# Kernel tuning notes

Measured on AMD Instinct MI355X. Metric: run time of the kernel, lower is better.

The kernel has to match this reference:

```python
import jax, jax.numpy as jnp
import numpy as np

N, E, IN_DIM, H, D, EDGE_DIM, T = 50000, 800000, 128, 4, 32, 32, 8
NEG_SLOPE = 0.2


def setup_inputs() -> dict:
    key = jax.random.key(0)
    ks = jax.random.split(key, 12)
    s = 0.1  # xavier-ish scale
    return {
        "h": jax.random.normal(ks[0], (N, IN_DIM), jnp.float32),
        "W": jax.random.normal(ks[1], (IN_DIM, D * H), jnp.float32) * s,
        "edge_emb": jax.random.normal(ks[2], (T, EDGE_DIM), jnp.float32) * s,
        "W_r": jax.random.normal(ks[3], (T, EDGE_DIM, EDGE_DIM * H), jnp.float32) * s,
        "a_l": jax.random.normal(ks[4], (1, H, D), jnp.float32) * s,
        "a_r": jax.random.normal(ks[5], (1, H, D), jnp.float32) * s,
        "a_e": jax.random.normal(ks[6], (1, H, EDGE_DIM), jnp.float32) * s,
        "res_w": jax.random.normal(ks[7], (IN_DIM, D * H), jnp.float32) * s,
        "res_b": jnp.zeros((D * H,), jnp.float32),
        "row": jax.random.randint(ks[8], (E,), 0, N),  # src node per edge
        "col": jax.random.randint(ks[9], (E,), 0, N),  # dst node per edge
        "etype": jax.random.randint(ks[10], (E,), 0, T),
    }


def reference(h, W, edge_emb, W_r, a_l, a_r, a_e, res_w, res_b, row, col, etype):
    # node projection: [N, H, D]
    emb = (h @ W).reshape(-1, H, D)

    # TypedLinear on edge-type embeddings. Since edge features depend only on
    # etype, compute the per-type result once, then gather per edge.
    e_t = jnp.einsum('te,tef->tf', edge_emb, W_r).reshape(T, H, EDGE_DIM)
    h_e_t = (a_e * e_t).sum(-1)            # [T, H]

    h_l = (a_l * emb).sum(-1)              # [N, H]
    h_r = (a_r * emb).sum(-1)              # [N, H]
    scores = h_l[row] + h_r[col] + h_e_t[etype]          # [E, H]
    scores = jax.nn.leaky_relu(scores, NEG_SLOPE)

    # segment softmax over edges sharing the same destination node (col)
    m = jax.ops.segment_max(scores, col, num_segments=N)  # [N, H]
    ex = jnp.exp(scores - m[col])
    denom = jax.ops.segment_sum(ex, col, num_segments=N)
    alpha = ex / denom[col]                # [E, H]

    # u_mul_e + scatter-sum to destination nodes
    msg = emb[row] * alpha[:, :, None]     # [E, H, D]
    agg = jax.ops.segment_sum(msg, col, num_segments=N)   # [N, H, D]

    # original permutes to [N, D, H] before flattening (d-major layout)
    out = jnp.transpose(agg, (0, 2, 1)).reshape(-1, D * H)
    out = out + h @ res_w + res_b          # residual
    return jax.nn.elu(out)
```

## Files before the change

kernel.cpp:

```cpp
#include <hip/hip_runtime.h>
#include <math.h>

#define NH 4
#define EDIM 32
#define NEG_SLOPE 0.2f
#define BSH 6
#define BCAP 2048

typedef __attribute__((ext_vector_type(8))) short short8;
typedef __attribute__((ext_vector_type(4))) float f32x4;
typedef __attribute__((ext_vector_type(2))) float f32x2;

__device__ __forceinline__ unsigned short f2bf(float f) {
    unsigned int x = __builtin_bit_cast(unsigned int, f);
    unsigned int r = (x + 0x7fffu + ((x >> 16) & 1u)) >> 16;
    return (unsigned short)r;
}
__device__ __forceinline__ float bf2f(unsigned short u) {
    unsigned int x = ((unsigned int)u) << 16;
    return __builtin_bit_cast(float, x);
}

__global__ __launch_bounds__(256) void k_prep(
    const float* __restrict__ W, const float* __restrict__ Rw,
    unsigned short* __restrict__ Wt, unsigned short* __restrict__ Rwt,
    int* __restrict__ bucket_cursor,
    const float* __restrict__ edge_emb, const float* __restrict__ W_r,
    const float* __restrict__ a_e, float* __restrict__ h_e_t)
{
    int tid = threadIdx.x;
    if (blockIdx.x < 64) {
        int idx = blockIdx.x * 256 + tid;
        int n = idx >> 7, k = idx & 127;
        Wt[n * 128 + k]  = f2bf(W[k * 128 + n]);
        Rwt[n * 128 + k] = f2bf(Rw[k * 128 + n]);
        if (idx < 1024) bucket_cursor[idx] = idx * BCAP;
    } else {
        int j = blockIdx.x - 64;
        int t = j >> 2;
        int ec = (j & 3) * 2 + (tid >> 7);
        int rem = tid & 127;
        float v = 0.f;
#pragma unroll
        for (int u = 0; u < 4; ++u) {
            int e = ec * 4 + u;
            v += edge_emb[t * EDIM + e] * W_r[(size_t)(t * EDIM + e) * 128 + rem];
        }
        v *= a_e[rem];
#pragma unroll
        for (int off = 16; off >= 1; off >>= 1)
            v += __shfl_xor(v, off);
        if ((rem & 31) == 0) atomicAdd(&h_e_t[t * NH + (rem >> 5)], v);
    }
}

__global__ __launch_bounds__(256) void k_gemm_fill(
    const float* __restrict__ A, const unsigned short* __restrict__ Wt,
    const unsigned short* __restrict__ Rwt, const float* __restrict__ Rb,
    const float* __restrict__ a_l, const float* __restrict__ a_r,
    unsigned short* __restrict__ EmbBf, unsigned short* __restrict__ ResBf,
    float* __restrict__ h_l, float* __restrict__ h_r, int M,
    const int* __restrict__ row, const int* __restrict__ col,
    const int* __restrict__ etype, int* __restrict__ bucket_cursor,
    unsigned* __restrict__ ebuf, int E, int NB, int nFill)
{
    __shared__ char lds[49152];
    int tid = threadIdx.x;

    if ((int)blockIdx.x < nFill) {
        int* bins = (int*)lds;
        int* base = bins + 1024;
        for (int i = tid; i < NB; i += 256) bins[i] = 0;
        __syncthreads();
        int lo = blockIdx.x * 8192;
        int ccol[32];
#pragma unroll
        for (int u = 0; u < 32; ++u) {
            int i = lo + tid + u * 256;
            int c = (i < E) ? col[i] : -1;
            ccol[u] = c;
            if (c >= 0) atomicAdd(&bins[c >> BSH], 1);
        }
        __syncthreads();
        for (int i = tid; i < NB; i += 256) {
            int c = bins[i];
            base[i] = c ? atomicAdd(&bucket_cursor[i], c) : 0;
            bins[i] = 0;
        }
        __syncthreads();
#pragma unroll
        for (int u = 0; u < 32; ++u) {
            int i = lo + tid + u * 256;
            int c = ccol[u];
            if (c >= 0) {
                int bk = c >> BSH;
                int p = base[bk] + atomicAdd(&bins[bk], 1);
                ebuf[p] = (unsigned)row[i] | ((unsigned)etype[i] << 16)
                        | ((unsigned)(c & 63) << 24);
            }
        }
        return;
    }

    int m0 = ((int)blockIdx.x - nFill) * 64;
#pragma unroll
    for (int i = 0; i < 4; ++i) {
        int c = tid + 256 * i;
        int r = c >> 4, kc = c & 15;
        int grow = m0 + r;
        float4 v0 = make_float4(0.f, 0.f, 0.f, 0.f), v1 = v0;
        if (grow < M) {
            v0 = *(const float4*)&A[(size_t)grow * 128 + kc * 8];
            v1 = *(const float4*)&A[(size_t)grow * 128 + kc * 8 + 4];
        }
        union { unsigned short u[8]; uint4 v; } p;
        p.u[0] = f2bf(v0.x); p.u[1] = f2bf(v0.y); p.u[2] = f2bf(v0.z); p.u[3] = f2bf(v0.w);
        p.u[4] = f2bf(v1.x); p.u[5] = f2bf(v1.y); p.u[6] = f2bf(v1.z); p.u[7] = f2bf(v1.w);
        int b = (r * 256 + kc * 16) ^ ((r & 7) << 4);
        *(uint4*)&lds[b] = p.v;
    }
#pragma unroll
    for (int i = 0; i < 8; ++i) {
        int c = tid + 256 * i;
        int n = c >> 4, kc = c & 15;
        uint4 v = *(const uint4*)&Wt[n * 128 + kc * 8];
        int b = 16384 + ((n * 256 + kc * 16) ^ ((n & 7) << 4));
        *(uint4*)&lds[b] = v;
    }
    __syncthreads();

    int w = tid >> 6, lane = tid & 63;
    int g = lane >> 4, l15 = lane & 15;
    int lrow = w * 16 + l15;

    short8 a[4];
#pragma unroll
    for (int s = 0; s < 4; ++s)
        a[s] = *(const short8*)&lds[(lrow * 256 + s * 64 + g * 16) ^ ((lrow & 7) << 4)];

    f32x4 acc[8];
#pragma unroll
    for (int f = 0; f < 8; ++f) acc[f] = (f32x4){0.f, 0.f, 0.f, 0.f};

#pragma unroll
    for (int f = 0; f < 8; ++f) {
        int n = f * 16 + l15;
        int nsw = (n & 7) << 4;
#pragma unroll
        for (int s = 0; s < 4; ++s) {
            short8 b = *(const short8*)&lds[16384 + ((n * 256 + s * 64 + g * 16) ^ nsw)];
            acc[f] = __builtin_amdgcn_mfma_f32_16x16x32_bf16(a[s], b, acc[f], 0, 0, 0);
        }
    }
#pragma unroll
    for (int f = 0; f < 8; ++f) {
        int col2 = f * 16 + l15;
#pragma unroll
        for (int reg = 0; reg < 4; ++reg) {
            int grow = m0 + w * 16 + g * 4 + reg;
            if (grow < M) EmbBf[(size_t)grow * 128 + col2] = f2bf(acc[f][reg]);
        }
    }
    {
        float alv[8], arv[8];
#pragma unroll
        for (int f = 0; f < 8; ++f) {
            alv[f] = a_l[f * 16 + l15];
            arv[f] = a_r[f * 16 + l15];
        }
#pragma unroll
        for (int reg = 0; reg < 4; ++reg) {
            float4 hl4, hr4;
#pragma unroll
            for (int hh = 0; hh < 4; ++hh) {
                float pl = alv[2 * hh] * acc[2 * hh][reg] + alv[2 * hh + 1] * acc[2 * hh + 1][reg];
                float pr = arv[2 * hh] * acc[2 * hh][reg] + arv[2 * hh + 1] * acc[2 * hh + 1][reg];
#pragma unroll
                for (int off = 8; off >= 1; off >>= 1) {
                    pl += __shfl_xor(pl, off);
                    pr += __shfl_xor(pr, off);
                }
                (&hl4.x)[hh] = pl;
                (&hr4.x)[hh] = pr;
            }
            int grow = m0 + w * 16 + g * 4 + reg;
            if (l15 == 0 && grow < M) {
                *(float4*)&h_l[(size_t)grow * 4] = hl4;
                *(float4*)&h_r[(size_t)grow * 4] = hr4;
            }
        }
    }

    __syncthreads();
#pragma unroll
    for (int i = 0; i < 8; ++i) {
        int c = tid + 256 * i;
        int n = c >> 4, kc = c & 15;
        uint4 v = *(const uint4*)&Rwt[n * 128 + kc * 8];
        int b = 16384 + ((n * 256 + kc * 16) ^ ((n & 7) << 4));
        *(uint4*)&lds[b] = v;
    }
    __syncthreads();

#pragma unroll
    for (int f = 0; f < 8; ++f) acc[f] = (f32x4){0.f, 0.f, 0.f, 0.f};
#pragma unroll
    for (int f = 0; f < 8; ++f) {
        int n = f * 16 + l15;
        int nsw = (n & 7) << 4;
#pragma unroll
        for (int s = 0; s < 4; ++s) {
            short8 b = *(const short8*)&lds[16384 + ((n * 256 + s * 64 + g * 16) ^ nsw)];
            acc[f] = __builtin_amdgcn_mfma_f32_16x16x32_bf16(a[s], b, acc[f], 0, 0, 0);
        }
    }
#pragma unroll
    for (int f = 0; f < 8; ++f) {
        int col2 = f * 16 + l15;
        float bias = Rb[col2];
#pragma unroll
        for (int reg = 0; reg < 4; ++reg) {
            int grow = m0 + w * 16 + g * 4 + reg;
            if (grow < M) ResBf[(size_t)grow * 128 + col2] = f2bf(acc[f][reg] + bias);
        }
    }
}

__global__ __launch_bounds__(512) void k_sort_aggregate(
    const unsigned* __restrict__ ebuf, const int* __restrict__ bucket_cursor,
    const float* __restrict__ h_l, const float* __restrict__ h_e_t,
    const float* __restrict__ h_r, const unsigned short* __restrict__ embBf,
    const unsigned short* __restrict__ resBf, float* __restrict__ out, int N)
{
    __shared__ int sedge[BCAP];
    __shared__ int cnt[64];
    __shared__ int scn[65];
    __shared__ char shalpha[8 * 1536];

    int b = blockIdx.x;
    int tid = threadIdx.x;
    int seg = b * BCAP;
    int m = bucket_cursor[b] - seg;

    if (tid < 64) cnt[tid] = 0;
    __syncthreads();
    for (int i = tid; i < m; i += 512)
        atomicAdd(&cnt[(ebuf[seg + i] >> 24) & 63], 1);
    __syncthreads();
    if (tid < 64) {
        int v = cnt[tid];
        int s = v;
#pragma unroll
        for (int off = 1; off < 64; off <<= 1) {
            int u2 = __shfl_up(s, off);
            if (tid >= off) s += u2;
        }
        scn[tid + 1] = s;
        if (tid == 0) scn[0] = 0;
        cnt[tid] = s - v;
    }
    __syncthreads();
    for (int i = tid; i < m; i += 512) {
        unsigned e = ebuf[seg + i];
        int p = atomicAdd(&cnt[(e >> 24) & 63], 1);
        sedge[p] = (int)(e & 0x00FFFFFFu);
    }
    __syncthreads();

    int w = tid >> 6, lane = tid & 63;
    int myh = lane >> 4;
    char* wb = &shalpha[w * 1536];
    const char* ab = wb + 256 + myh * 260;
    const char* embByte = (const char*)embBf;

    for (int it = 0; it < 8; ++it) {
        int nd = it * 8 + w;
        int n = b * 64 + nd;
        if (n >= N) break;
        int st0 = scn[nd];
        int deg = scn[nd + 1] - st0;
        float4 hrv = *(const float4*)&h_r[(size_t)n * 4];
        f32x2 acc2 = (f32x2){0.f, 0.f};

        if (deg <= 64) {
            bool act = lane < deg;
            float p0 = 0.f, p1 = 0.f, p2 = 0.f, p3 = 0.f;
            if (act) {
                int pk = sedge[st0 + lane];
                int r = pk & 0xffff;
                float4 hl = *(const float4*)&h_l[(size_t)r * 4];
                float4 he = *(const float4*)&h_e_t[(size_t)(pk >> 16) * 4];
                float sc0 = hl.x + he.x + hrv.x; sc0 = sc0 > 0.f ? sc0 : NEG_SLOPE * sc0;
                float sc1 = hl.y + he.y + hrv.y; sc1 = sc1 > 0.f ? sc1 : NEG_SLOPE * sc1;
                float sc2 = hl.z + he.z + hrv.z; sc2 = sc2 > 0.f ? sc2 : NEG_SLOPE * sc2;
                float sc3 = hl.w + he.w + hrv.w; sc3 = sc3 > 0.f ? sc3 : NEG_SLOPE * sc3;
                p0 = __expf(sc0); p1 = __expf(sc1);
                p2 = __expf(sc2); p3 = __expf(sc3);
                *(int*)(wb + lane * 4) = pk << 8 >> 8 << 8;
                *(int*)(wb + lane * 4) = (pk & 0xffff) << 8;
                *(float*)(wb + 256 + 0 * 260 + lane * 4) = p0;
                *(float*)(wb + 256 + 1 * 260 + lane * 4) = p1;
                *(float*)(wb + 256 + 2 * 260 + lane * 4) = p2;
                *(float*)(wb + 256 + 3 * 260 + lane * 4) = p3;
            }
            float d0 = p0, d1 = p1, d2 = p2, d3 = p3;
#pragma unroll
            for (int off = 32; off >= 1; off >>= 1) {
                d0 += __shfl_xor(d0, off); d1 += __shfl_xor(d1, off);
                d2 += __shfl_xor(d2, off); d3 += __shfl_xor(d3, off);
            }
            float den = myh == 0 ? d0 : myh == 1 ? d1 : myh == 2 ? d2 : d3;
            float inv = (deg > 0) ? __builtin_amdgcn_rcpf(den) : 0.f;

            int q = 0;
            for (; q + 8 <= deg; q += 8) {
                int ro[8]; float aq[8];
#pragma unroll
                for (int u = 0; u < 8; ++u) ro[u] = *(const int*)(wb + (q + u) * 4);
#pragma unroll
                for (int u = 0; u < 8; ++u) aq[u] = *(const float*)(ab + (q + u) * 4);
                unsigned int ev[8];
#pragma unroll
                for (int u = 0; u < 8; ++u)
                    ev[u] = *(const unsigned int*)(embByte + (size_t)(unsigned)(ro[u] + lane * 4));
#pragma unroll
                for (int u = 0; u < 8; ++u) {
                    f32x2 ef;
                    ef.x = __builtin_bit_cast(float, ev[u] << 16);
                    ef.y = __builtin_bit_cast(float, ev[u] & 0xffff0000u);
                    acc2 = __builtin_elementwise_fma(ef, (f32x2){aq[u], aq[u]}, acc2);
                }
            }
            for (; q < deg; ++q) {
                int ro = *(const int*)(wb + q * 4);
                float aq = *(const float*)(ab + q * 4);
                unsigned int ev = *(const unsigned int*)(embByte + (size_t)(unsigned)(ro + lane * 4));
                f32x2 ef;
                ef.x = __builtin_bit_cast(float, ev << 16);
                ef.y = __builtin_bit_cast(float, ev & 0xffff0000u);
                acc2 = __builtin_elementwise_fma(ef, (f32x2){aq, aq}, acc2);
            }
            acc2.x *= inv; acc2.y *= inv;
        } else {
            float d0 = 0.f, d1 = 0.f, d2 = 0.f, d3 = 0.f;
            for (int base2 = 0; base2 < deg; base2 += 64) {
                int el = base2 + lane;
                if (el < deg) {
                    int pk = sedge[st0 + el];
                    float4 hl = *(const float4*)&h_l[(size_t)(pk & 0xffff) * 4];
                    float4 he = *(const float4*)&h_e_t[(size_t)(pk >> 16) * 4];
                    float sc0 = hl.x + he.x + hrv.x; sc0 = sc0 > 0.f ? sc0 : NEG_SLOPE * sc0;
                    float sc1 = hl.y + he.y + hrv.y; sc1 = sc1 > 0.f ? sc1 : NEG_SLOPE * sc1;
                    float sc2 = hl.z + he.z + hrv.z; sc2 = sc2 > 0.f ? sc2 : NEG_SLOPE * sc2;
                    float sc3 = hl.w + he.w + hrv.w; sc3 = sc3 > 0.f ? sc3 : NEG_SLOPE * sc3;
                    d0 += __expf(sc0); d1 += __expf(sc1);
                    d2 += __expf(sc2); d3 += __expf(sc3);
                }
            }
#pragma unroll
            for (int off = 32; off >= 1; off >>= 1) {
                d0 += __shfl_xor(d0, off); d1 += __shfl_xor(d1, off);
                d2 += __shfl_xor(d2, off); d3 += __shfl_xor(d3, off);
            }
            float den = myh == 0 ? d0 : myh == 1 ? d1 : myh == 2 ? d2 : d3;
            float inv = __builtin_amdgcn_rcpf(den);
            for (int base2 = 0; base2 < deg; base2 += 64) {
                int el = base2 + lane;
                float p0 = 0.f, p1 = 0.f, p2 = 0.f, p3 = 0.f;
                int r = 0;
                if (el < deg) {
                    int pk = sedge[st0 + el];
                    r = pk & 0xffff;
                    float4 hl = *(const float4*)&h_l[(size_t)r * 4];
                    float4 he = *(const float4*)&h_e_t[(size_t)(pk >> 16) * 4];
                    float sc0 = hl.x + he.x + hrv.x; sc0 = sc0 > 0.f ? sc0 : NEG_SLOPE * sc0;
                    float sc1 = hl.y + he.y + hrv.y; sc1 = sc1 > 0.f ? sc1 : NEG_SLOPE * sc1;
                    float sc2 = hl.z + he.z + hrv.z; sc2 = sc2 > 0.f ? sc2 : NEG_SLOPE * sc2;
                    float sc3 = hl.w + he.w + hrv.w; sc3 = sc3 > 0.f ? sc3 : NEG_SLOPE * sc3;
                    p0 = __expf(sc0); p1 = __expf(sc1);
                    p2 = __expf(sc2); p3 = __expf(sc3);
                }
                int cmax = (deg - base2 < 64) ? (deg - base2) : 64;
                for (int qq = 0; qq < cmax; ++qq) {
                    int rq = __shfl(r, qq);
                    float a0 = __shfl(p0, qq), a1 = __shfl(p1, qq);
                    float a2 = __shfl(p2, qq), a3 = __shfl(p3, qq);
                    float aq = myh == 0 ? a0 : myh == 1 ? a1 : myh == 2 ? a2 : a3;
                    unsigned int ev = *(const unsigned int*)&embBf[(size_t)rq * 128 + lane * 2];
                    f32x2 ef;
                    ef.x = __builtin_bit_cast(float, ev << 16);
                    ef.y = __builtin_bit_cast(float, ev & 0xffff0000u);
                    acc2 = __builtin_elementwise_fma(ef, (f32x2){aq, aq}, acc2);
                }
            }
            acc2.x *= inv; acc2.y *= inv;
        }

        int j0 = lane * 2;
        int h0 = j0 >> 5, dd0 = j0 & 31;
        size_t ob = (size_t)n * 128;
        float o0 = acc2.x + bf2f(resBf[ob + dd0 * 4 + h0]);
        float o1 = acc2.y + bf2f(resBf[ob + (dd0 + 1) * 4 + h0]);
        out[ob + dd0 * 4 + h0] = o0 > 0.f ? o0 : expm1f(o0);
        out[ob + (dd0 + 1) * 4 + h0] = o1 > 0.f ? o1 : expm1f(o1);
    }
}

extern "C" void kernel_launch(void* const* d_in, const int* in_sizes, int n_in,
                              void* d_out, int out_size, void* d_ws, size_t ws_size,
                              hipStream_t stream)
{
    const float* h        = (const float*)d_in[0];
    const float* W        = (const float*)d_in[1];
    const float* edge_emb = (const float*)d_in[2];
    const float* W_r      = (const float*)d_in[3];
    const float* a_l      = (const float*)d_in[4];
    const float* a_r      = (const float*)d_in[5];
    const float* a_e      = (const float*)d_in[6];
    const float* res_w    = (const float*)d_in[7];
    const float* res_b    = (const float*)d_in[8];
    const int*   row      = (const int*)d_in[9];
    const int*   col      = (const int*)d_in[10];
    const int*   etype    = (const int*)d_in[11];
    float* out = (float*)d_out;

    int N = in_sizes[0] / 128;
    int E = in_sizes[9];
    int T = in_sizes[2] / EDIM;
    int NB = (N + 63) >> BSH;

    char* ws = (char*)d_ws;
    size_t off = 0;
    auto alloc = [&](size_t bytes) -> char* {
        char* p = ws + off;
        off = (off + bytes + 255) & ~(size_t)255;
        return p;
    };
    unsigned short* embBf = (unsigned short*)alloc((size_t)N * 128 * 2);
    unsigned short* resBf = (unsigned short*)alloc((size_t)N * 128 * 2);
    unsigned short* Wt    = (unsigned short*)alloc((size_t)128 * 128 * 2);
    unsigned short* Rwt   = (unsigned short*)alloc((size_t)128 * 128 * 2);
    float* h_l   = (float*)alloc((size_t)N * 4 * 4);
    float* h_r   = (float*)alloc((size_t)N * 4 * 4);
    float* h_e_t = (float*)alloc((size_t)T * 4 * 4);
    int* bucket_cursor = (int*)alloc(1024 * 4);
    unsigned* ebuf = (unsigned*)alloc((size_t)(NB + 1) * BCAP * 4);

    int nFill = (E + 8191) / 8192;
    int nGemm = (N + 63) / 64;

    hipMemsetAsync(h_e_t, 0, (size_t)T * NH * 4, stream);
    hipLaunchKernelGGL(k_prep, dim3(64 + T * 4), dim3(256), 0, stream,
                       W, res_w, Wt, Rwt, bucket_cursor,
                       edge_emb, W_r, a_e, h_e_t);
    hipLaunchKernelGGL(k_gemm_fill, dim3(nFill + nGemm), dim3(256), 0, stream,
                       h, Wt, Rwt, res_b, a_l, a_r, embBf, resBf, h_l, h_r, N,
                       row, col, etype, bucket_cursor, ebuf, E, NB, nFill);
    hipLaunchKernelGGL(k_sort_aggregate, dim3(NB), dim3(512), 0, stream,
                       ebuf, bucket_cursor, h_l, h_e_t, h_r, embBf, resBf, out, N);
}
```

Measured before the change: 91.89 us.

## Halve bucket size and split edge gather across half-waves with 8-byte loads

```diff
diff --git a/kernel.cpp b/kernel.cpp
--- a/kernel.cpp
+++ b/kernel.cpp
@@ -4,8 +4,8 @@
 #define NH 4
 #define EDIM 32
 #define NEG_SLOPE 0.2f
-#define BSH 6
-#define BCAP 2048
+#define BSH 5
+#define BCAP 1024
 
 typedef __attribute__((ext_vector_type(8))) short short8;
 typedef __attribute__((ext_vector_type(4))) float f32x4;
@@ -34,7 +34,7 @@
         int n = idx >> 7, k = idx & 127;
         Wt[n * 128 + k]  = f2bf(W[k * 128 + n]);
         Rwt[n * 128 + k] = f2bf(Rw[k * 128 + n]);
-        if (idx < 1024) bucket_cursor[idx] = idx * BCAP;
+        if (idx < 2048) bucket_cursor[idx] = idx * BCAP;
     } else {
         int j = blockIdx.x - 64;
         int t = j >> 2;
@@ -69,13 +69,13 @@
 
     if ((int)blockIdx.x < nFill) {
         int* bins = (int*)lds;
-        int* base = bins + 1024;
+        int* base = bins + 2048;
         for (int i = tid; i < NB; i += 256) bins[i] = 0;
         __syncthreads();
-        int lo = blockIdx.x * 8192;
-        int ccol[32];
-#pragma unroll
-        for (int u = 0; u < 32; ++u) {
+        int lo = blockIdx.x * 4096;
+        int ccol[16];
+#pragma unroll
+        for (int u = 0; u < 16; ++u) {
             int i = lo + tid + u * 256;
             int c = (i < E) ? col[i] : -1;
             ccol[u] = c;
@@ -89,14 +89,14 @@
         }
         __syncthreads();
 #pragma unroll
-        for (int u = 0; u < 32; ++u) {
+        for (int u = 0; u < 16; ++u) {
             int i = lo + tid + u * 256;
             int c = ccol[u];
             if (c >= 0) {
                 int bk = c >> BSH;
                 int p = base[bk] + atomicAdd(&bins[bk], 1);
                 ebuf[p] = (unsigned)row[i] | ((unsigned)etype[i] << 16)
-                        | ((unsigned)(c & 63) << 24);
+                        | ((unsigned)(c & 31) << 24);
             }
         }
         return;
@@ -226,32 +226,32 @@
     }
 }
 
-__global__ __launch_bounds__(512) void k_sort_aggregate(
+__global__ __launch_bounds__(256) void k_sort_aggregate(
     const unsigned* __restrict__ ebuf, const int* __restrict__ bucket_cursor,
     const float* __restrict__ h_l, const float* __restrict__ h_e_t,
     const float* __restrict__ h_r, const unsigned short* __restrict__ embBf,
     const unsigned short* __restrict__ resBf, float* __restrict__ out, int N)
 {
     __shared__ int sedge[BCAP];
-    __shared__ int cnt[64];
-    __shared__ int scn[65];
-    __shared__ char shalpha[8 * 1536];
+    __shared__ int cnt[32];
+    __shared__ int scn[33];
+    __shared__ char shalpha[4 * 1536];
 
     int b = blockIdx.x;
     int tid = threadIdx.x;
     int seg = b * BCAP;
     int m = bucket_cursor[b] - seg;
 
-    if (tid < 64) cnt[tid] = 0;
-    __syncthreads();
-    for (int i = tid; i < m; i += 512)
-        atomicAdd(&cnt[(ebuf[seg + i] >> 24) & 63], 1);
-    __syncthreads();
-    if (tid < 64) {
+    if (tid < 32) cnt[tid] = 0;
+    __syncthreads();
+    for (int i = tid; i < m; i += 256)
+        atomicAdd(&cnt[(ebuf[seg + i] >> 24) & 31], 1);
+    __syncthreads();
+    if (tid < 32) {
         int v = cnt[tid];
         int s = v;
 #pragma unroll
-        for (int off = 1; off < 64; off <<= 1) {
+        for (int off = 1; off < 32; off <<= 1) {
             int u2 = __shfl_up(s, off);
             if (tid >= off) s += u2;
         }
@@ -260,27 +260,29 @@
         cnt[tid] = s - v;
     }
     __syncthreads();
-    for (int i = tid; i < m; i += 512) {
+    for (int i = tid; i < m; i += 256) {
         unsigned e = ebuf[seg + i];
-        int p = atomicAdd(&cnt[(e >> 24) & 63], 1);
+        int p = atomicAdd(&cnt[(e >> 24) & 31], 1);
         sedge[p] = (int)(e & 0x00FFFFFFu);
     }
     __syncthreads();
 
     int w = tid >> 6, lane = tid & 63;
     int myh = lane >> 4;
+    int l31 = lane & 31;
+    int hq = l31 >> 3;
+    int sel = lane >> 5;
     char* wb = &shalpha[w * 1536];
-    const char* ab = wb + 256 + myh * 260;
+    const char* ab2 = wb + 256 + hq * 260;
     const char* embByte = (const char*)embBf;
 
     for (int it = 0; it < 8; ++it) {
-        int nd = it * 8 + w;
-        int n = b * 64 + nd;
+        int nd = it * 4 + w;
+        int n = b * 32 + nd;
         if (n >= N) break;
         int st0 = scn[nd];
         int deg = scn[nd + 1] - st0;
         float4 hrv = *(const float4*)&h_r[(size_t)n * 4];
-        f32x2 acc2 = (f32x2){0.f, 0.f};
 
         if (deg <= 64) {
             bool act = lane < deg;
@@ -296,7 +298,6 @@
                 float sc3 = hl.w + he.w + hrv.w; sc3 = sc3 > 0.f ? sc3 : NEG_SLOPE * sc3;
                 p0 = __expf(sc0); p1 = __expf(sc1);
                 p2 = __expf(sc2); p3 = __expf(sc3);
-                *(int*)(wb + lane * 4) = pk << 8 >> 8 << 8;
                 *(int*)(wb + lane * 4) = (pk & 0xffff) << 8;
                 *(float*)(wb + 256 + 0 * 260 + lane * 4) = p0;
                 *(float*)(wb + 256 + 1 * 260 + lane * 4) = p1;
@@ -309,39 +310,53 @@
                 d0 += __shfl_xor(d0, off); d1 += __shfl_xor(d1, off);
                 d2 += __shfl_xor(d2, off); d3 += __shfl_xor(d3, off);
             }
-            float den = myh == 0 ? d0 : myh == 1 ? d1 : myh == 2 ? d2 : d3;
+            float den = hq == 0 ? d0 : hq == 1 ? d1 : hq == 2 ? d2 : d3;
             float inv = (deg > 0) ? __builtin_amdgcn_rcpf(den) : 0.f;
 
-            int q = 0;
-            for (; q + 8 <= deg; q += 8) {
-                int ro[8]; float aq[8];
-#pragma unroll
-                for (int u = 0; u < 8; ++u) ro[u] = *(const int*)(wb + (q + u) * 4);
-#pragma unroll
-                for (int u = 0; u < 8; ++u) aq[u] = *(const float*)(ab + (q + u) * 4);
-                unsigned int ev[8];
-#pragma unroll
-                for (int u = 0; u < 8; ++u)
-                    ev[u] = *(const unsigned int*)(embByte + (size_t)(unsigned)(ro[u] + lane * 4));
-#pragma unroll
-                for (int u = 0; u < 8; ++u) {
-                    f32x2 ef;
-                    ef.x = __builtin_bit_cast(float, ev[u] << 16);
-                    ef.y = __builtin_bit_cast(float, ev[u] & 0xffff0000u);
-                    acc2 = __builtin_elementwise_fma(ef, (f32x2){aq[u], aq[u]}, acc2);
-                }
-            }
-            for (; q < deg; ++q) {
-                int ro = *(const int*)(wb + q * 4);
-                float aq = *(const float*)(ab + q * 4);
-                unsigned int ev = *(const unsigned int*)(embByte + (size_t)(unsigned)(ro + lane * 4));
-                f32x2 ef;
-                ef.x = __builtin_bit_cast(float, ev << 16);
-                ef.y = __builtin_bit_cast(float, ev & 0xffff0000u);
-                acc2 = __builtin_elementwise_fma(ef, (f32x2){aq, aq}, acc2);
-            }
-            acc2.x *= inv; acc2.y *= inv;
+            f32x4 acc4 = (f32x4){0.f, 0.f, 0.f, 0.f};
+            for (int q = 0; q < deg; q += 8) {
+                unsigned ro[4]; float aq[4];
+#pragma unroll
+                for (int u = 0; u < 4; ++u) {
+                    int qe = q + 2 * u + sel;
+                    int qc = qe < deg ? qe : deg - 1;
+                    ro[u] = *(const unsigned*)(wb + qc * 4);
+                    float av = *(const float*)(ab2 + qc * 4);
+                    aq[u] = (qe < deg) ? av : 0.f;
+                }
+                uint2 ev[4];
+#pragma unroll
+                for (int u = 0; u < 4; ++u)
+                    ev[u] = *(const uint2*)(embByte + (size_t)(ro[u] + l31 * 8));
+#pragma unroll
+                for (int u = 0; u < 4; ++u) {
+                    f32x4 ef;
+                    ef.x = __builtin_bit_cast(float, ev[u].x << 16);
+                    ef.y = __builtin_bit_cast(float, ev[u].x & 0xffff0000u);
+                    ef.z = __builtin_bit_cast(float, ev[u].y << 16);
+                    ef.w = __builtin_bit_cast(float, ev[u].y & 0xffff0000u);
+                    acc4 = __builtin_elementwise_fma(
+                        ef, (f32x4){aq[u], aq[u], aq[u], aq[u]}, acc4);
+                }
+            }
+            acc4.x += __shfl_xor(acc4.x, 32);
+            acc4.y += __shfl_xor(acc4.y, 32);
+            acc4.z += __shfl_xor(acc4.z, 32);
+            acc4.w += __shfl_xor(acc4.w, 32);
+
+            if (lane < 32) {
+                size_t ob = (size_t)n * 128;
+                int bj = lane * 4;
+                int h0 = bj >> 5;
+#pragma unroll
+                for (int u = 0; u < 4; ++u) {
+                    int d = (bj + u) & 31;
+                    float o = acc4[u] * inv + bf2f(resBf[ob + d * 4 + h0]);
+                    out[ob + d * 4 + h0] = o > 0.f ? o : expm1f(o);
+                }
+            }
         } else {
+            f32x2 acc2 = (f32x2){0.f, 0.f};
             float d0 = 0.f, d1 = 0.f, d2 = 0.f, d3 = 0.f;
             for (int base2 = 0; base2 < deg; base2 += 64) {
                 int el = base2 + lane;
@@ -385,24 +400,22 @@
                     int rq = __shfl(r, qq);
                     float a0 = __shfl(p0, qq), a1 = __shfl(p1, qq);
                     float a2 = __shfl(p2, qq), a3 = __shfl(p3, qq);
-                    float aq = myh == 0 ? a0 : myh == 1 ? a1 : myh == 2 ? a2 : a3;
+                    float aqv = myh == 0 ? a0 : myh == 1 ? a1 : myh == 2 ? a2 : a3;
                     unsigned int ev = *(const unsigned int*)&embBf[(size_t)rq * 128 + lane * 2];
                     f32x2 ef;
                     ef.x = __builtin_bit_cast(float, ev << 16);
                     ef.y = __builtin_bit_cast(float, ev & 0xffff0000u);
-                    acc2 = __builtin_elementwise_fma(ef, (f32x2){aq, aq}, acc2);
-                }
-            }
-            acc2.x *= inv; acc2.y *= inv;
-        }
-
-        int j0 = lane * 2;
-        int h0 = j0 >> 5, dd0 = j0 & 31;
-        size_t ob = (size_t)n * 128;
-        float o0 = acc2.x + bf2f(resBf[ob + dd0 * 4 + h0]);
-        float o1 = acc2.y + bf2f(resBf[ob + (dd0 + 1) * 4 + h0]);
-        out[ob + dd0 * 4 + h0] = o0 > 0.f ? o0 : expm1f(o0);
-        out[ob + (dd0 + 1) * 4 + h0] = o1 > 0.f ? o1 : expm1f(o1);
+                    acc2 = __builtin_elementwise_fma(ef, (f32x2){aqv, aqv}, acc2);
+                }
+            }
+            int j0 = lane * 2;
+            int h0 = j0 >> 5, dd0 = j0 & 31;
+            size_t ob = (size_t)n * 128;
+            float o0 = acc2.x * inv + bf2f(resBf[ob + dd0 * 4 + h0]);
+            float o1 = acc2.y * inv + bf2f(resBf[ob + (dd0 + 1) * 4 + h0]);
+            out[ob + dd0 * 4 + h0] = o0 > 0.f ? o0 : expm1f(o0);
+            out[ob + (dd0 + 1) * 4 + h0] = o1 > 0.f ? o1 : expm1f(o1);
+        }
     }
 }
 
@@ -427,7 +440,7 @@
     int N = in_sizes[0] / 128;
     int E = in_sizes[9];
     int T = in_sizes[2] / EDIM;
-    int NB = (N + 63) >> BSH;
+    int NB = (N + 31) >> BSH;
 
     char* ws = (char*)d_ws;
     size_t off = 0;
@@ -443,10 +456,10 @@
     float* h_l   = (float*)alloc((size_t)N * 4 * 4);
     float* h_r   = (float*)alloc((size_t)N * 4 * 4);
     float* h_e_t = (float*)alloc((size_t)T * 4 * 4);
-    int* bucket_cursor = (int*)alloc(1024 * 4);
+    int* bucket_cursor = (int*)alloc(2048 * 4);
     unsigned* ebuf = (unsigned*)alloc((size_t)(NB + 1) * BCAP * 4);
 
-    int nFill = (E + 8191) / 8192;
+    int nFill = (E + 4095) / 4096;
     int nGemm = (N + 63) / 64;
 
     hipMemsetAsync(h_e_t, 0, (size_t)T * NH * 4, stream);
@@ -456,6 +469,6 @@
     hipLaunchKernelGGL(k_gemm_fill, dim3(nFill + nGemm), dim3(256), 0, stream,
                        h, Wt, Rwt, res_b, a_l, a_r, embBf, resBf, h_l, h_r, N,
                        row, col, etype, bucket_cursor, ebuf, E, NB, nFill);
-    hipLaunchKernelGGL(k_sort_aggregate, dim3(NB), dim3(512), 0, stream,
+    hipLaunchKernelGGL(k_sort_aggregate, dim3(NB), dim3(256), 0, stream,
                        ebuf, bucket_cursor, h_l, h_e_t, h_r, embBf, resBf, out, N);
 }
```

New measurement: 94.22 us. 2.5% more time.
